# Kernel tuning notes

Hardware: AMD Instinct MI355X
Metric: run time of the kernel (lower is better)

Reference implementation:

```python
import jax, jax.numpy as jnp
import numpy as np

B, T, E = 4, 2048, 1024
H = 16
QK_SQUEEZE = 2
S = E // QK_SQUEEZE          # squeeze_dim = 512
SHD = S // H                 # squeeze_head_dim = 32
HD = E // H                  # head_dim = 64
SCALING = SHD ** -0.5


def setup_inputs() -> dict:
    key = jax.random.key(0)
    ks = jax.random.split(key, 9)
    def w(k, shape, fan_in):
        return jax.random.normal(k, shape, jnp.float32) * (fan_in ** -0.5)
    return {
        "hidden_states": jax.random.normal(ks[0], (B, T, E), jnp.float32),
        "Wq": w(ks[1], (E, S), E), "bq": jnp.zeros((S,), jnp.float32),
        "Wk": w(ks[2], (E, S), E), "bk": jnp.zeros((S,), jnp.float32),
        "Wv": w(ks[3], (E, E), E), "bv": jnp.zeros((E,), jnp.float32),
        "Wo": w(ks[4], (E, E), E), "bo": jnp.zeros((E,), jnp.float32),
    }


def reference(hidden_states, Wq, bq, Wk, bk, Wv, bv, Wo, bo):
    # Projections; Q pre-scaled as in the torch module.
    q = ((hidden_states @ Wq + bq) * SCALING).reshape(B, T, H, SHD)
    k = (hidden_states @ Wk + bk).reshape(B, T, H, SHD)
    v = (hidden_states @ Wv + bv).reshape(B, T, H, HD)
    # [B, H, Tq, Tk] attention logits with squeezed head dim.
    attn = jnp.einsum("bqhd,bkhd->bhqk", q, k)
    p = jax.nn.softmax(attn, axis=-1)  # dropout p=0.0 -> identity
    out = jnp.einsum("bhqk,bkhd->bqhd", p, v).reshape(B, T, E)
    return out @ Wo + bo
```

## Files before the change

### kernel.cpp

```cpp
#include <hip/hip_runtime.h>
#include <stdint.h>


#define QSCALE (0.17677669529663687f * 1.4426950408889634f)

typedef __bf16 bf16x8 __attribute__((ext_vector_type(8)));
typedef float f32x4 __attribute__((ext_vector_type(4)));
typedef float f32x8 __attribute__((ext_vector_type(8)));
typedef float f32x16 __attribute__((ext_vector_type(16)));
typedef unsigned int u32x2 __attribute__((ext_vector_type(2)));
typedef unsigned int u32x4v __attribute__((ext_vector_type(4)));

static __device__ __forceinline__ unsigned short f2b(float f) {
  return __builtin_bit_cast(unsigned short, (__bf16)f);
}
static __device__ __forceinline__ unsigned int cvtpk(float lo, float hi) {
  unsigned int r;
  asm("v_cvt_pk_bf16_f32 %0, %1, %2" : "=v"(r) : "v"(lo), "v"(hi));
  return r;
}
static __device__ __forceinline__ void gl_lds16(const void* g, void* s) {
  __builtin_amdgcn_global_load_lds(
      (const __attribute__((address_space(1))) unsigned int*)(uintptr_t)g,
      (__attribute__((address_space(3))) unsigned int*)(uintptr_t)s, 16, 0, 0);
}
static __device__ __forceinline__ void pswap(unsigned int& a, unsigned int& b) {
#if __has_builtin(__builtin_amdgcn_permlane32_swap)
  u32x2 r = __builtin_amdgcn_permlane32_swap(a, b, false, false);
  a = r.x;
  b = r.y;
#else
  asm("v_permlane32_swap_b32 %0, %1" : "+v"(a), "+v"(b));
#endif
}

__global__ void k_cvt_hs(const float* __restrict__ in, unsigned short* __restrict__ out) {
  int i = (blockIdx.x * 256 + threadIdx.x) * 4;
  float4 v = *(const float4*)(in + i);
  ushort4 u = make_ushort4(f2b(v.x), f2b(v.y), f2b(v.z), f2b(v.w));
  *(ushort4*)(out + i) = u;
}

__global__ void k_cvt_wT(const float* __restrict__ W, unsigned short* __restrict__ WT,
                         int N, float scale) {
  __shared__ float tile[64][65];
  const int kt = blockIdx.x & 15;
  const int nt = blockIdx.x >> 4;
  const int k0 = kt * 64, n0 = nt * 64;
  const int t = threadIdx.x;
  {
    int kl = t >> 2, c = t & 3;
    const float* src = W + (size_t)(k0 + kl) * N + n0 + c * 16;
#pragma unroll
    for (int j = 0; j < 4; j++) {
      float4 v = *(const float4*)(src + j * 4);
      tile[kl][c * 16 + j * 4 + 0] = v.x;
      tile[kl][c * 16 + j * 4 + 1] = v.y;
      tile[kl][c * 16 + j * 4 + 2] = v.z;
      tile[kl][c * 16 + j * 4 + 3] = v.w;
    }
  }
  __syncthreads();
  {
    int nl = t >> 2, c2 = t & 3;
    unsigned short us[16];
#pragma unroll
    for (int j = 0; j < 16; j++) us[j] = f2b(tile[c2 * 16 + j][nl] * scale);
    uint4 a, b;
    a.x = (unsigned)us[0] | ((unsigned)us[1] << 16);
    a.y = (unsigned)us[2] | ((unsigned)us[3] << 16);
    a.z = (unsigned)us[4] | ((unsigned)us[5] << 16);
    a.w = (unsigned)us[6] | ((unsigned)us[7] << 16);
    b.x = (unsigned)us[8] | ((unsigned)us[9] << 16);
    b.y = (unsigned)us[10] | ((unsigned)us[11] << 16);
    b.z = (unsigned)us[12] | ((unsigned)us[13] << 16);
    b.w = (unsigned)us[14] | ((unsigned)us[15] << 16);
    unsigned short* dst = WT + (size_t)(n0 + nl) * 1024 + k0 + c2 * 16;
    *(uint4*)dst = a;
    *(uint4*)(dst + 8) = b;
  }
}

__global__ void k_bias(const float* __restrict__ bq, const float* __restrict__ bk,
                       const float* __restrict__ bv, float* __restrict__ bqkv) {
  int n = blockIdx.x * 256 + threadIdx.x;
  float v;
  if (n < 512) v = bq[n] * QSCALE;
  else if (n < 1024) v = bk[n - 512];
  else v = bv[n - 1024];
  bqkv[n] = v;
}

__global__ __launch_bounds__(512, 2) void k_gemm256qkv(
    const unsigned short* __restrict__ A, const unsigned short* __restrict__ BT,
    const float* __restrict__ bias,
    unsigned short* __restrict__ qo, unsigned short* __restrict__ ko,
    unsigned short* __restrict__ vo) {
  __shared__ alignas(128) char smem[131072];
  const int tid = threadIdx.x;
  const int w = tid >> 6, l = tid & 63, lm = l & 15, lc = l >> 4;
  const int wm = w >> 2, wn = w & 3;
  const int mt = blockIdx.x & 31, nt = blockIdx.x >> 5;
  const int brow = mt << 8, bcol = nt << 8;

  f32x4 acc[8][4] = {};

  auto stage = [&](int kt, int buf) {
    const unsigned short* As = A + (size_t)brow * 1024 + kt * 64;
    const unsigned short* Bs = BT + (size_t)bcol * 1024 + kt * 64;
    char* la = smem + buf * 32768;
    char* lb = smem + 65536 + buf * 32768;
#pragma unroll
    for (int j = 0; j < 4; j++) {
      const int p = j * 512 + tid;
      const int r = p >> 3;
      const int cc = (p & 7) ^ (r & 7);
      gl_lds16(As + (size_t)r * 1024 + cc * 8, la + (j * 512 + w * 64) * 16);
      gl_lds16(Bs + (size_t)r * 1024 + cc * 8, lb + (j * 512 + w * 64) * 16);
    }
  };

  stage(0, 0);
  stage(1, 1);
  asm volatile("s_waitcnt vmcnt(8)" ::: "memory");
  __builtin_amdgcn_s_barrier();
  __builtin_amdgcn_sched_barrier(0);

#pragma unroll 2
  for (int t = 0; t < 16; ++t) {
    const char* la = smem + (t & 1) * 32768;
    const char* lb = smem + 65536 + (t & 1) * 32768;
#pragma unroll
    for (int kk = 0; kk < 2; kk++) {
      const int csw = kk * 64 + lc * 16;
      bf16x8 af[8], bf[4];
#pragma unroll
      for (int mi = 0; mi < 8; mi++)
        af[mi] = *(const bf16x8*)(la + (wm * 128 + mi * 16 + lm) * 128 +
                                  (csw ^ ((lm & 7) << 4)));
#pragma unroll
      for (int ni = 0; ni < 4; ni++)
        bf[ni] = *(const bf16x8*)(lb + (wn * 64 + ni * 16 + lm) * 128 +
                                  (csw ^ ((lm & 7) << 4)));
      __builtin_amdgcn_s_setprio(1);
#pragma unroll
      for (int mi = 0; mi < 8; mi++)
#pragma unroll
        for (int ni = 0; ni < 4; ni++)
          acc[mi][ni] = __builtin_amdgcn_mfma_f32_16x16x32_bf16(af[mi], bf[ni],
                                                                acc[mi][ni], 0, 0, 0);
      __builtin_amdgcn_s_setprio(0);
    }
    asm volatile("s_waitcnt lgkmcnt(0)" ::: "memory");
    __builtin_amdgcn_sched_barrier(0);
    __builtin_amdgcn_s_barrier();
    if (t + 2 < 16) {
      stage(t + 2, t & 1);
      asm volatile("s_waitcnt vmcnt(8)" ::: "memory");
    } else {
      asm volatile("s_waitcnt vmcnt(0)" ::: "memory");
    }
    __builtin_amdgcn_s_barrier();
    __builtin_amdgcn_sched_barrier(0);
  }

#pragma unroll
  for (int nf = 0; nf < 4; nf++) {
    const int n = bcol + wn * 64 + nf * 16 + lm;
    const float bv_ = bias[n];
#pragma unroll
    for (int mf = 0; mf < 8; mf++) {
      const int m0 = brow + wm * 128 + mf * 16 + lc * 4;
      f32x4 v = acc[mf][nf];
      const float x0 = v[0] + bv_, x1 = v[1] + bv_, x2 = v[2] + bv_, x3 = v[3] + bv_;
      const int b = m0 >> 11, t0 = m0 & 2047;
      if (n < 1024) {
        unsigned short* dst = (n < 512) ? qo : ko;
        const int nn = n & 511, h = nn >> 5, d = nn & 31;
        const size_t base = ((size_t)((b << 4) + h) * 2048 + t0) * 32 + d;
        dst[base + 0 * 32] = f2b(x0);
        dst[base + 1 * 32] = f2b(x1);
        dst[base + 2 * 32] = f2b(x2);
        dst[base + 3 * 32] = f2b(x3);
      } else {
        const int e = n - 1024, h = e >> 6, hd = e & 63;
        ushort4 u = make_ushort4(f2b(x0), f2b(x1), f2b(x2), f2b(x3));
        *(ushort4*)(vo + (((size_t)((b << 4) + h) * 256 + (t0 >> 3)) * 64 + hd) * 8 +
                    (t0 & 7)) = u;
      }
    }
  }
}

template <int MODE>
__global__ __launch_bounds__(256) void k_gemm(
    const unsigned short* __restrict__ A, const unsigned short* __restrict__ BT,
    const float* __restrict__ bias, int M, int N,
    unsigned short* __restrict__ qo, unsigned short* __restrict__ ko,
    unsigned short* __restrict__ vo, float* __restrict__ fo) {
  constexpr int K = 1024;
  __shared__ alignas(128) char smem[16384];
  const int tid = threadIdx.x;
  const int w = tid >> 6, l = tid & 63, lm = l & 15, lc = l >> 4;
  const int nmt = M >> 7;
  const int mt = blockIdx.x % nmt, nt = blockIdx.x / nmt;
  const int brow = mt << 7, bcol = nt << 7;
  const int wm = w >> 1, wn = w & 1;
  f32x4 acc[4][4] = {};
  const int ca = w * 64 + l;

  for (int k0 = 0; k0 < K; k0 += 32) {
#pragma unroll
    for (int j = 0; j < 2; j++) {
      int c = j * 256 + ca;
      gl_lds16(A + (size_t)(brow + (c >> 2)) * K + k0 + (c & 3) * 8,
               smem + (j * 256 + w * 64) * 16);
      gl_lds16(BT + (size_t)(bcol + (c >> 2)) * K + k0 + (c & 3) * 8,
               smem + 8192 + (j * 256 + w * 64) * 16);
    }
    __syncthreads();
    bf16x8 af[4], bf[4];
#pragma unroll
    for (int i = 0; i < 4; i++) {
      af[i] = *(const bf16x8*)(smem + (wm * 64 + i * 16 + lm) * 64 + lc * 16);
      bf[i] = *(const bf16x8*)(smem + 8192 + (wn * 64 + i * 16 + lm) * 64 + lc * 16);
    }
#pragma unroll
    for (int ai = 0; ai < 4; ai++)
#pragma unroll
      for (int bj = 0; bj < 4; bj++)
        acc[ai][bj] = __builtin_amdgcn_mfma_f32_16x16x32_bf16(af[ai], bf[bj], acc[ai][bj], 0, 0, 0);
    __syncthreads();
  }

#pragma unroll
  for (int bj = 0; bj < 4; bj++) {
    const int n = bcol + wn * 64 + bj * 16 + lm;
    const float bv_ = bias[n];
#pragma unroll
    for (int ai = 0; ai < 4; ai++) {
      const int m0 = brow + wm * 64 + ai * 16 + lc * 4;
      f32x4 v = acc[ai][bj];
      const float x0 = v[0] + bv_, x1 = v[1] + bv_, x2 = v[2] + bv_, x3 = v[3] + bv_;
      if constexpr (MODE == 0) {
        const int b = m0 >> 11, t0 = m0 & 2047;
        if (n < 1024) {
          unsigned short* dst = (n < 512) ? qo : ko;
          const int nn = n & 511, h = nn >> 5, d = nn & 31;
          const size_t base = ((size_t)((b << 4) + h) * 2048 + t0) * 32 + d;
          dst[base + 0 * 32] = f2b(x0);
          dst[base + 1 * 32] = f2b(x1);
          dst[base + 2 * 32] = f2b(x2);
          dst[base + 3 * 32] = f2b(x3);
        } else {
          const int e = n - 1024, h = e >> 6, hd = e & 63;
          ushort4 u = make_ushort4(f2b(x0), f2b(x1), f2b(x2), f2b(x3));
          *(ushort4*)(vo + (((size_t)((b << 4) + h) * 256 + (t0 >> 3)) * 64 + hd) * 8 +
                      (t0 & 7)) = u;
        }
      } else {
        float* dst = fo + (size_t)m0 * N + n;
        dst[0 * N] = x0;
        dst[1 * N] = x1;
        dst[2 * N] = x2;
        dst[3 * N] = x3;
      }
    }
  }
}

__global__ __launch_bounds__(128, 2) void k_attn6(
    const unsigned short* __restrict__ qb, const unsigned short* __restrict__ kb,
    const unsigned short* __restrict__ v3, unsigned short* __restrict__ aout) {
  __shared__ float red[64][67];
  const int tid = threadIdx.x, kvh = tid >> 6, l = tid & 63;
  const int l31 = l & 31, hf = l >> 5;
  const int xcd = blockIdx.x & 7, slot = blockIdx.x >> 3;
  const int bh = xcd + ((slot >> 5) << 3);
  const int qrow0 = (slot & 31) << 6;

  const unsigned short* qrow = qb + ((size_t)bh * 2048 + qrow0 + l31) * 32 + hf * 8;
  const bf16x8 qA0 = *(const bf16x8*)(qrow);
  const bf16x8 qA1 = *(const bf16x8*)(qrow + 16);
  const bf16x8 qB0 = *(const bf16x8*)(qrow + 1024);
  const bf16x8 qB1 = *(const bf16x8*)(qrow + 1024 + 16);

  const unsigned short* kp = kb + ((size_t)bh * 2048 + kvh * 1024 + l31) * 32 + hf * 8;
  const unsigned short* vp = v3 + (((size_t)bh * 256 + kvh * 128 + hf) * 64 + l31) * 8;

  f32x16 oA0 = {}, oA1 = {}, oB0 = {}, oB1 = {};
  f32x4 lsA4 = {}, lsB4 = {};

  auto tile_body = [&](bf16x8 kf0, bf16x8 kf1, bf16x8 va00, bf16x8 va01, bf16x8 va10,
                       bf16x8 va11) {
    f32x16 sA = {}, sB = {};
    sA = __builtin_amdgcn_mfma_f32_32x32x16_bf16(kf0, qA0, sA, 0, 0, 0);
    sA = __builtin_amdgcn_mfma_f32_32x32x16_bf16(kf1, qA1, sA, 0, 0, 0);
    sB = __builtin_amdgcn_mfma_f32_32x32x16_bf16(kf0, qB0, sB, 0, 0, 0);
    sB = __builtin_amdgcn_mfma_f32_32x32x16_bf16(kf1, qB1, sB, 0, 0, 0);

#pragma unroll
    for (int i = 0; i < 16; i++) sA[i] = __builtin_amdgcn_exp2f(sA[i]);
#pragma unroll
    for (int i = 0; i < 16; i++) sB[i] = __builtin_amdgcn_exp2f(sB[i]);
    {
      f32x8 t8 = __builtin_shufflevector(sA, sA, 0, 1, 2, 3, 4, 5, 6, 7) +
                 __builtin_shufflevector(sA, sA, 8, 9, 10, 11, 12, 13, 14, 15);
      lsA4 += __builtin_shufflevector(t8, t8, 0, 1, 2, 3) +
              __builtin_shufflevector(t8, t8, 4, 5, 6, 7);
    }
    {
      f32x8 t8 = __builtin_shufflevector(sB, sB, 0, 1, 2, 3, 4, 5, 6, 7) +
                 __builtin_shufflevector(sB, sB, 8, 9, 10, 11, 12, 13, 14, 15);
      lsB4 += __builtin_shufflevector(t8, t8, 0, 1, 2, 3) +
              __builtin_shufflevector(t8, t8, 4, 5, 6, 7);
    }
    unsigned int pa[8], pb[8];
#pragma unroll
    for (int i = 0; i < 8; i++) pa[i] = cvtpk(sA[2 * i], sA[2 * i + 1]);
#pragma unroll
    for (int i = 0; i < 8; i++) pb[i] = cvtpk(sB[2 * i], sB[2 * i + 1]);
    pswap(pa[0], pa[2]);
    pswap(pa[1], pa[3]);
    pswap(pa[4], pa[6]);
    pswap(pa[5], pa[7]);
    pswap(pb[0], pb[2]);
    pswap(pb[1], pb[3]);
    pswap(pb[4], pb[6]);
    pswap(pb[5], pb[7]);
    const bf16x8 fA0 = __builtin_bit_cast(bf16x8, (u32x4v){pa[0], pa[1], pa[2], pa[3]});
    const bf16x8 fA1 = __builtin_bit_cast(bf16x8, (u32x4v){pa[4], pa[5], pa[6], pa[7]});
    const bf16x8 fB0 = __builtin_bit_cast(bf16x8, (u32x4v){pb[0], pb[1], pb[2], pb[3]});
    const bf16x8 fB1 = __builtin_bit_cast(bf16x8, (u32x4v){pb[4], pb[5], pb[6], pb[7]});

    __builtin_amdgcn_s_setprio(1);
    oA0 = __builtin_amdgcn_mfma_f32_32x32x16_bf16(va00, fA0, oA0, 0, 0, 0);
    oA1 = __builtin_amdgcn_mfma_f32_32x32x16_bf16(va01, fA0, oA1, 0, 0, 0);
    oB0 = __builtin_amdgcn_mfma_f32_32x32x16_bf16(va00, fB0, oB0, 0, 0, 0);
    oB1 = __builtin_amdgcn_mfma_f32_32x32x16_bf16(va01, fB0, oB1, 0, 0, 0);
    oA0 = __builtin_amdgcn_mfma_f32_32x32x16_bf16(va10, fA1, oA0, 0, 0, 0);
    oA1 = __builtin_amdgcn_mfma_f32_32x32x16_bf16(va11, fA1, oA1, 0, 0, 0);
    oB0 = __builtin_amdgcn_mfma_f32_32x32x16_bf16(va10, fB1, oB0, 0, 0, 0);
    oB1 = __builtin_amdgcn_mfma_f32_32x32x16_bf16(va11, fB1, oB1, 0, 0, 0);
    __builtin_amdgcn_s_setprio(0);
  };

  bf16x8 kf0 = *(const bf16x8*)(kp);
  bf16x8 kf1 = *(const bf16x8*)(kp + 16);
  bf16x8 va00 = *(const bf16x8*)(vp + 0);
  bf16x8 va01 = *(const bf16x8*)(vp + 256);
  bf16x8 va10 = *(const bf16x8*)(vp + 1024);
  bf16x8 va11 = *(const bf16x8*)(vp + 1280);

  for (int it = 0; it < 31; ++it) {
    kp += 1024;
    vp += 2048;
    const bf16x8 nk0 = *(const bf16x8*)(kp);
    const bf16x8 nk1 = *(const bf16x8*)(kp + 16);
    const bf16x8 nv00 = *(const bf16x8*)(vp + 0);
    const bf16x8 nv01 = *(const bf16x8*)(vp + 256);
    const bf16x8 nv10 = *(const bf16x8*)(vp + 1024);
    const bf16x8 nv11 = *(const bf16x8*)(vp + 1280);

    tile_body(kf0, kf1, va00, va01, va10, va11);

    kf0 = nk0;
    kf1 = nk1;
    va00 = nv00;
    va01 = nv01;
    va10 = nv10;
    va11 = nv11;
  }
  tile_body(kf0, kf1, va00, va01, va10, va11);

  float lsA = (lsA4[0] + lsA4[1]) + (lsA4[2] + lsA4[3]);
  float lsB = (lsB4[0] + lsB4[1]) + (lsB4[2] + lsB4[3]);
  lsA += __shfl_xor(lsA, 32);
  lsB += __shfl_xor(lsB, 32);

  if (kvh == 1) {
    float* r = &red[l][0];
#pragma unroll
    for (int i = 0; i < 16; i++) {
      r[i] = oA0[i];
      r[16 + i] = oA1[i];
      r[32 + i] = oB0[i];
      r[48 + i] = oB1[i];
    }
    r[64] = lsA;
    r[65] = lsB;
  }
  __syncthreads();
  if (kvh == 0) {
    const float* r = &red[l][0];
#pragma unroll
    for (int i = 0; i < 16; i++) {
      oA0[i] += r[i];
      oA1[i] += r[16 + i];
      oB0[i] += r[32 + i];
      oB1[i] += r[48 + i];
    }
    lsA += r[64];
    lsB += r[65];

    const int b = bh >> 4, hh = bh & 15;
    const float rA = 1.0f / lsA, rB = 1.0f / lsB;
    unsigned short* orowA = aout + ((size_t)(b * 2048 + qrow0 + l31)) * 1024 + hh * 64;
    unsigned short* orowB = orowA + (size_t)32 * 1024;
#pragma unroll
    for (int hc = 0; hc < 2; hc++) {
#pragma unroll
      for (int rg = 0; rg < 4; rg++) {
        const f32x16& oa = hc ? oA1 : oA0;
        ushort4 ua = make_ushort4(f2b(oa[rg * 4 + 0] * rA), f2b(oa[rg * 4 + 1] * rA),
                                  f2b(oa[rg * 4 + 2] * rA), f2b(oa[rg * 4 + 3] * rA));
        *(ushort4*)(orowA + hc * 32 + rg * 8 + hf * 4) = ua;
        const f32x16& ob = hc ? oB1 : oB0;
        ushort4 ub = make_ushort4(f2b(ob[rg * 4 + 0] * rB), f2b(ob[rg * 4 + 1] * rB),
                                  f2b(ob[rg * 4 + 2] * rB), f2b(ob[rg * 4 + 3] * rB));
        *(ushort4*)(orowB + hc * 32 + rg * 8 + hf * 4) = ub;
      }
    }
  }
}

extern "C" void kernel_launch(void* const* d_in, const int* in_sizes, int n_in,
                              void* d_out, int out_size, void* d_ws, size_t ws_size,
                              hipStream_t stream) {
  const float* hs = (const float*)d_in[0];
  const float* Wq = (const float*)d_in[1];
  const float* bq = (const float*)d_in[2];
  const float* Wk = (const float*)d_in[3];
  const float* bk = (const float*)d_in[4];
  const float* Wv = (const float*)d_in[5];
  const float* bv = (const float*)d_in[6];
  const float* Wo = (const float*)d_in[7];
  const float* bo = (const float*)d_in[8];

  char* ws = (char*)d_ws;
  unsigned short* hsb   = (unsigned short*)(ws + 0);
  unsigned short* wqkvT = (unsigned short*)(ws + 16777216);
  unsigned short* woT   = (unsigned short*)(ws + 20971520);
  float*          bqkv  = (float*)        (ws + 23068672);
  unsigned short* qbuf  = (unsigned short*)(ws + 23076864);
  unsigned short* kbuf  = (unsigned short*)(ws + 31465472);
  unsigned short* vTb   = (unsigned short*)(ws + 39854080);
  unsigned short* aoutb = (unsigned short*)(ws + 56631296);

  k_cvt_hs<<<8192, 256, 0, stream>>>(hs, hsb);
  k_cvt_wT<<<128, 256, 0, stream>>>(Wq, wqkvT, 512, QSCALE);
  k_cvt_wT<<<128, 256, 0, stream>>>(Wk, wqkvT + 512 * 1024, 512, 1.0f);
  k_cvt_wT<<<256, 256, 0, stream>>>(Wv, wqkvT + 1024 * 1024, 1024, 1.0f);
  k_cvt_wT<<<256, 256, 0, stream>>>(Wo, woT, 1024, 1.0f);
  k_bias<<<8, 256, 0, stream>>>(bq, bk, bv, bqkv);

  k_gemm256qkv<<<256, 512, 0, stream>>>(hsb, wqkvT, bqkv, qbuf, kbuf, vTb);
  k_attn6<<<2048, 128, 0, stream>>>(qbuf, kbuf, vTb, aoutb);
  k_gemm<1><<<64 * 8, 256, 0, stream>>>(aoutb, woT, bo, 8192, 1024,
                                        nullptr, nullptr, nullptr, (float*)d_out);
}
```

Baseline: 154.7 us.

## Replace output projection GEMM with double-buffered 256x128 tiled kernel

The generic 128x128 output-projection GEMM, which had a single LDS buffer and synchronous K loop, is replaced by a dedicated kernel using 256x128 tiles, 512 threads, and K-step 64. The new kernel double-buffers global-to-LDS loads with explicit waitcnt and barriers, so loads overlap MFMA work. It also XOR-swizzles the LDS layout to avoid bank conflicts. The larger tiles and 96KB of LDS per block mean fewer blocks (256) and lower occupancy, and only 256 blocks run across the CUs.

```diff
diff --git a/kernel.cpp b/kernel.cpp
--- a/kernel.cpp
+++ b/kernel.cpp
@@ -192,79 +192,96 @@
   }
 }
 
-template <int MODE>
-__global__ __launch_bounds__(256) void k_gemm(
+__global__ __launch_bounds__(512, 2) void k_gemm256o(
     const unsigned short* __restrict__ A, const unsigned short* __restrict__ BT,
-    const float* __restrict__ bias, int M, int N,
-    unsigned short* __restrict__ qo, unsigned short* __restrict__ ko,
-    unsigned short* __restrict__ vo, float* __restrict__ fo) {
-  constexpr int K = 1024;
-  __shared__ alignas(128) char smem[16384];
+    const float* __restrict__ bias, float* __restrict__ fo) {
+  __shared__ alignas(128) char smem[98304];
   const int tid = threadIdx.x;
   const int w = tid >> 6, l = tid & 63, lm = l & 15, lc = l >> 4;
-  const int nmt = M >> 7;
-  const int mt = blockIdx.x % nmt, nt = blockIdx.x / nmt;
-  const int brow = mt << 7, bcol = nt << 7;
-  const int wm = w >> 1, wn = w & 1;
-  f32x4 acc[4][4] = {};
-  const int ca = w * 64 + l;
-
-  for (int k0 = 0; k0 < K; k0 += 32) {
+  const int wm = w >> 2, wn = w & 3;
+  const int mt = blockIdx.x & 31, nt = blockIdx.x >> 5;
+  const int brow = mt << 8, bcol = nt << 7;
+
+  f32x4 acc[8][2] = {};
+
+  auto stage = [&](int kt, int buf) {
+    const unsigned short* As = A + (size_t)brow * 1024 + kt * 64;
+    const unsigned short* Bs = BT + (size_t)bcol * 1024 + kt * 64;
+    char* la = smem + buf * 32768;
+    char* lb = smem + 65536 + buf * 16384;
+#pragma unroll
+    for (int j = 0; j < 4; j++) {
+      const int p = j * 512 + tid;
+      const int r = p >> 3;
+      const int cc = (p & 7) ^ (r & 7);
+      gl_lds16(As + (size_t)r * 1024 + cc * 8, la + (j * 512 + w * 64) * 16);
+    }
 #pragma unroll
     for (int j = 0; j < 2; j++) {
-      int c = j * 256 + ca;
-      gl_lds16(A + (size_t)(brow + (c >> 2)) * K + k0 + (c & 3) * 8,
-               smem + (j * 256 + w * 64) * 16);
-      gl_lds16(BT + (size_t)(bcol + (c >> 2)) * K + k0 + (c & 3) * 8,
-               smem + 8192 + (j * 256 + w * 64) * 16);
-    }
-    __syncthreads();
-    bf16x8 af[4], bf[4];
-#pragma unroll
-    for (int i = 0; i < 4; i++) {
-      af[i] = *(const bf16x8*)(smem + (wm * 64 + i * 16 + lm) * 64 + lc * 16);
-      bf[i] = *(const bf16x8*)(smem + 8192 + (wn * 64 + i * 16 + lm) * 64 + lc * 16);
-    }
-#pragma unroll
-    for (int ai = 0; ai < 4; ai++)
-#pragma unroll
-      for (int bj = 0; bj < 4; bj++)
-        acc[ai][bj] = __builtin_amdgcn_mfma_f32_16x16x32_bf16(af[ai], bf[bj], acc[ai][bj], 0, 0, 0);
-    __syncthreads();
-  }
-
-#pragma unroll
-  for (int bj = 0; bj < 4; bj++) {
-    const int n = bcol + wn * 64 + bj * 16 + lm;
+      const int p = j * 512 + tid;
+      const int r = p >> 3;
+      const int cc = (p & 7) ^ (r & 7);
+      gl_lds16(Bs + (size_t)r * 1024 + cc * 8, lb + (j * 512 + w * 64) * 16);
+    }
+  };
+
+  stage(0, 0);
+  stage(1, 1);
+  asm volatile("s_waitcnt vmcnt(6)" ::: "memory");
+  __builtin_amdgcn_s_barrier();
+  __builtin_amdgcn_sched_barrier(0);
+
+#pragma unroll 2
+  for (int t = 0; t < 16; ++t) {
+    const char* la = smem + (t & 1) * 32768;
+    const char* lb = smem + 65536 + (t & 1) * 16384;
+#pragma unroll
+    for (int kk = 0; kk < 2; kk++) {
+      const int csw = kk * 64 + lc * 16;
+      bf16x8 af[8], bf[2];
+#pragma unroll
+      for (int mi = 0; mi < 8; mi++)
+        af[mi] = *(const bf16x8*)(la + (wm * 128 + mi * 16 + lm) * 128 +
+                                  (csw ^ ((lm & 7) << 4)));
+#pragma unroll
+      for (int ni = 0; ni < 2; ni++)
+        bf[ni] = *(const bf16x8*)(lb + (wn * 32 + ni * 16 + lm) * 128 +
+                                  (csw ^ ((lm & 7) << 4)));
+      __builtin_amdgcn_s_setprio(1);
+#pragma unroll
+      for (int mi = 0; mi < 8; mi++)
+#pragma unroll
+        for (int ni = 0; ni < 2; ni++)
+          acc[mi][ni] = __builtin_amdgcn_mfma_f32_16x16x32_bf16(af[mi], bf[ni],
+                                                                acc[mi][ni], 0, 0, 0);
+      __builtin_amdgcn_s_setprio(0);
+    }
+    asm volatile("s_waitcnt lgkmcnt(0)" ::: "memory");
+    __builtin_amdgcn_sched_barrier(0);
+    __builtin_amdgcn_s_barrier();
+    if (t + 2 < 16) {
+      stage(t + 2, t & 1);
+      asm volatile("s_waitcnt vmcnt(6)" ::: "memory");
+    } else {
+      asm volatile("s_waitcnt vmcnt(0)" ::: "memory");
+    }
+    __builtin_amdgcn_s_barrier();
+    __builtin_amdgcn_sched_barrier(0);
+  }
+
+#pragma unroll
+  for (int nf = 0; nf < 2; nf++) {
+    const int n = bcol + wn * 32 + nf * 16 + lm;
     const float bv_ = bias[n];
 #pragma unroll
-    for (int ai = 0; ai < 4; ai++) {
-      const int m0 = brow + wm * 64 + ai * 16 + lc * 4;
-      f32x4 v = acc[ai][bj];
-      const float x0 = v[0] + bv_, x1 = v[1] + bv_, x2 = v[2] + bv_, x3 = v[3] + bv_;
-      if constexpr (MODE == 0) {
-        const int b = m0 >> 11, t0 = m0 & 2047;
-        if (n < 1024) {
-          unsigned short* dst = (n < 512) ? qo : ko;
-          const int nn = n & 511, h = nn >> 5, d = nn & 31;
-          const size_t base = ((size_t)((b << 4) + h) * 2048 + t0) * 32 + d;
-          dst[base + 0 * 32] = f2b(x0);
-          dst[base + 1 * 32] = f2b(x1);
-          dst[base + 2 * 32] = f2b(x2);
-          dst[base + 3 * 32] = f2b(x3);
-        } else {
-          const int e = n - 1024, h = e >> 6, hd = e & 63;
-          ushort4 u = make_ushort4(f2b(x0), f2b(x1), f2b(x2), f2b(x3));
-          *(ushort4*)(vo + (((size_t)((b << 4) + h) * 256 + (t0 >> 3)) * 64 + hd) * 8 +
-                      (t0 & 7)) = u;
-        }
-      } else {
-        float* dst = fo + (size_t)m0 * N + n;
-        dst[0 * N] = x0;
-        dst[1 * N] = x1;
-        dst[2 * N] = x2;
-        dst[3 * N] = x3;
-      }
+    for (int mf = 0; mf < 8; mf++) {
+      const int m0 = brow + wm * 128 + mf * 16 + lc * 4;
+      f32x4 v = acc[mf][nf];
+      float* dst = fo + (size_t)m0 * 1024 + n;
+      dst[0 * 1024] = v[0] + bv_;
+      dst[1 * 1024] = v[1] + bv_;
+      dst[2 * 1024] = v[2] + bv_;
+      dst[3 * 1024] = v[3] + bv_;
     }
   }
 }
@@ -456,6 +473,5 @@
 
   k_gemm256qkv<<<256, 512, 0, stream>>>(hsb, wqkvT, bqkv, qbuf, kbuf, vTb);
   k_attn6<<<2048, 128, 0, stream>>>(qbuf, kbuf, vTb, aoutb);
-  k_gemm<1><<<64 * 8, 256, 0, stream>>>(aoutb, woT, bo, 8192, 1024,
-                                        nullptr, nullptr, nullptr, (float*)d_out);
-}
+  k_gemm256o<<<256, 512, 0, stream>>>(aoutb, woT, bo, (float*)d_out);
+}
```

After: 152.5 us. Within noise of the previous version (-1.4%).
